# Kernel optimization log

Hardware: AMD Instinct MI355X
Metric: run time of the kernel (lower is better)

Reference implementation:

```python
import jax, jax.numpy as jnp
import numpy as np

B, T, C, H, W = 32, 64, 2, 32, 32
NK, KS = 16, 6          # n_kernels, kernel_size
ACT = 27                # conv output spatial size (32-6+1)
FEAT = ACT * ACT * NK   # 11664 flattened features
RU = 16                 # rnn_units
AD_RATE_L, REC_RATE_L = 0.1, 0.1   # AdaptiveLayer rates
AD_RATE_R, REC_RATE_R = 0.4, 0.1   # SimpleRNN rates


def setup_inputs() -> dict:
    key = jax.random.key(0)
    ks = jax.random.split(key, 8)
    stdv = 1.0 / np.sqrt(RU)
    return {
        "x": jax.random.normal(ks[0], (B, T, C, H, W), jnp.float32),
        "conv_w": jax.random.normal(ks[1], (NK, C, KS, KS), jnp.float32) * 0.01,
        "conv_b": jnp.full((NK,), 0.01, jnp.float32),
        "w_ih": jax.random.uniform(ks[2], (RU, FEAT), jnp.float32, -stdv, stdv),
        "w_hh": jax.random.uniform(ks[3], (RU, RU), jnp.float32, -stdv, stdv),
        "b_ih": jax.random.uniform(ks[4], (RU,), jnp.float32, -stdv, stdv),
        "b_hh": jax.random.uniform(ks[5], (RU,), jnp.float32, -stdv, stdv),
        "fc_w": jax.random.normal(ks[6], (2, RU), jnp.float32) * 0.01,
        "fc_b": jnp.full((2,), 0.01, jnp.float32),
    }


def reference(x, conv_w, conv_b, w_ih, w_hh, b_ih, b_hh, fc_w, fc_b):
    Bn, Tn = x.shape[:2]
    # per-frame conv: fold frames into batch
    xf = x.reshape(Bn * Tn, C, H, W)
    conv = jax.lax.conv_general_dilated(
        xf, conv_w, window_strides=(1, 1), padding='VALID',
        dimension_numbers=('NCHW', 'OIHW', 'NCHW'))
    conv = conv + conv_b[None, :, None, None]
    out_conv = conv.reshape(Bn, Tn, NK, ACT, ACT)
    out_flat = jax.nn.relu(out_conv.reshape(Bn, Tn, FEAT))

    # AdaptiveLayer: per-frame clamp/decay scan (initial adaptation is zeros)
    def ad_step(adapt, frame):
        out = jnp.maximum(frame - adapt, 0.0)
        adapt = (adapt + AD_RATE_L * out) * (1.0 - REC_RATE_L)
        return adapt, out
    _, adapted = jax.lax.scan(ad_step, jnp.zeros((Bn, FEAT), x.dtype),
                              jnp.swapaxes(out_flat, 0, 1))
    out_adapted = jnp.swapaxes(adapted, 0, 1)  # [B,T,FEAT]

    # SimpleRNN with adaptation state
    def rnn_step(carry, x_t):
        h, adapt = carry
        pre = x_t @ w_ih.T + b_ih + h @ w_hh.T + b_hh
        a = jnp.maximum(pre - adapt, 0.0)
        adapt = (adapt + AD_RATE_R * a) * (1.0 - REC_RATE_R)
        h = jax.nn.relu(a)
        return (h, adapt), h
    h0 = jnp.zeros((Bn, RU), x.dtype)
    _, hs = jax.lax.scan(rnn_step, (h0, h0), jnp.swapaxes(out_adapted, 0, 1))
    out_rnn = jnp.swapaxes(hs, 0, 1)  # [B,T,RU]

    out_fc = out_rnn @ fc_w.T + fc_b  # [B,T,2]
    return (out_fc, out_conv, out_flat, out_rnn)
```

## Files before the change

kernel.cpp:

```cpp
#include <hip/hip_runtime.h>

#define FEAT 11664
#define OFF_FC   0u
#define OFF_CONV 4096u
#define OFF_FLAT 23891968u
#define OFF_RNN  47779840u

static __device__ __forceinline__ unsigned short f2bf(float f) {
    unsigned int u = __float_as_uint(f);
    u += 0x7FFFu + ((u >> 16) & 1u);
    return (unsigned short)(u >> 16);
}

__global__ __launch_bounds__(128) void k_conv(const float* __restrict__ x,
                                              const float* __restrict__ cw,
                                              const float* __restrict__ cb,
                                              float* __restrict__ out)
{
    __shared__ __align__(16) float smem[11664];
    __shared__ float bls[16];
    float* xs  = smem;
    float* wls = smem + 2304;
    float* ot  = smem;
    const int tid = threadIdx.x;
    const int frame = blockIdx.x;

    const float4* xg = (const float4*)(x + (size_t)frame * 2048);
    for (int c0 = tid; c0 < 512; c0 += 128) {
        float4 v = xg[c0];
        int e0 = c0 * 4;
        int ch = e0 >> 10, rem = e0 & 1023, row = rem >> 5, col = rem & 31;
        float* dst = &xs[ch * 1152 + row * 36 + col];
        dst[0] = v.x; dst[1] = v.y; dst[2] = v.z; dst[3] = v.w;
    }
    for (int idx = tid; idx < 1152; idx += 128) {
        int k = idx / 72;
        int rem = idx - k * 72;
        wls[rem * 16 + k] = cw[idx];
    }
    if (tid < 16) bls[tid] = cb[tid];
    __syncthreads();

    const int kg = tid >> 5;
    const int r  = tid & 31;
    float acc[4][27];
    if (r < 27) {
        #pragma unroll
        for (int kk = 0; kk < 4; ++kk)
            #pragma unroll
            for (int c = 0; c < 27; ++c) acc[kk][c] = 0.f;

        for (int ch = 0; ch < 2; ++ch) {
            for (int i = 0; i < 6; ++i) {
                const float* rowp = &xs[ch * 1152 + (r + i) * 36];
                float xr[32];
                #pragma unroll
                for (int m = 0; m < 8; ++m) {
                    float4 v = ((const float4*)rowp)[m];
                    xr[4*m+0] = v.x; xr[4*m+1] = v.y; xr[4*m+2] = v.z; xr[4*m+3] = v.w;
                }
                float4 wj[6];
                #pragma unroll
                for (int j = 0; j < 6; ++j)
                    wj[j] = *(const float4*)&wls[(ch * 36 + i * 6 + j) * 16 + kg * 4];
                #pragma unroll
                for (int j = 0; j < 6; ++j) {
                    #pragma unroll
                    for (int c = 0; c < 27; ++c) {
                        float xv = xr[c + j];
                        acc[0][c] = fmaf(xv, wj[j].x, acc[0][c]);
                        acc[1][c] = fmaf(xv, wj[j].y, acc[1][c]);
                        acc[2][c] = fmaf(xv, wj[j].z, acc[2][c]);
                        acc[3][c] = fmaf(xv, wj[j].w, acc[3][c]);
                    }
                }
            }
        }
    }

    __syncthreads();
    if (r < 27) {
        #pragma unroll
        for (int kk = 0; kk < 4; ++kk) {
            float bv = bls[kg * 4 + kk];
            float* dst = &ot[(kg * 4 + kk) * 729 + r * 27];
            #pragma unroll
            for (int c = 0; c < 27; ++c) dst[c] = acc[kk][c] + bv;
        }
    }
    __syncthreads();

    const float4* src4 = (const float4*)ot;
    float4* dc = (float4*)(out + OFF_CONV + (size_t)frame * FEAT);
    float4* df = (float4*)(out + OFF_FLAT + (size_t)frame * FEAT);
    for (int e = tid; e < 2916; e += 128) {
        float4 v = src4[e];
        dc[e] = v;
        float4 rv;
        rv.x = v.x > 0.f ? v.x : 0.f;
        rv.y = v.y > 0.f ? v.y : 0.f;
        rv.z = v.z > 0.f ? v.z : 0.f;
        rv.w = v.w > 0.f ? v.w : 0.f;
        df[e] = rv;
    }
}

typedef short bf16x8 __attribute__((ext_vector_type(8)));
typedef float f32x4  __attribute__((ext_vector_type(4)));

__global__ __launch_bounds__(256) void k_adapt_proj48(const float* __restrict__ flat,
                                                      const float* __restrict__ w_ih,
                                                      float* __restrict__ partial)
{
    __shared__ __align__(16) unsigned short A[16 * 264];
    __shared__ __align__(16) unsigned short Bw[16 * 264];
    __shared__ __align__(16) float accscr[4 * 64 * 4];
    const int tid = threadIdx.x;
    const int b  = blockIdx.x / 48;
    const int fb = blockIdx.x % 48;
    const int fbase = fb * 243;

    float v[16];
    if (tid < 243) {
        const float* p0 = flat + (size_t)(b * 64) * FEAT + fbase + tid;
        #pragma unroll
        for (int tl = 0; tl < 16; ++tl) v[tl] = p0[(size_t)tl * FEAT];
    }

    for (int n = 0; n < 16; ++n) {
        if (tid < 243) Bw[n * 264 + tid] = f2bf(w_ih[(size_t)n * FEAT + fbase + tid]);
    }
    if (tid < 208) {
        int n = tid / 13, c = 243 + tid % 13;
        A[n * 264 + c]  = 0;
        Bw[n * 264 + c] = 0;
    }
    __syncthreads();

    float ad = 0.f;
    const int w = tid >> 6, l = tid & 63;
    const int m = l & 15, q = l >> 4;

    for (int tt = 0; tt < 4; ++tt) {
        if (tid < 243) {
            unsigned short* arow = &A[tid];
            #pragma unroll
            for (int tl = 0; tl < 16; ++tl) {
                float o = fmaxf(v[tl] - ad, 0.f); ad = (ad + 0.1f * o) * 0.9f;
                arow[tl * 264] = f2bf(o);
            }
        }
        __syncthreads();

        if (tt < 3 && tid < 243) {
            const float* pn = flat + (size_t)(b * 64 + (tt + 1) * 16) * FEAT + fbase + tid;
            #pragma unroll
            for (int tl = 0; tl < 16; ++tl) v[tl] = pn[(size_t)tl * FEAT];
        }

        f32x4 acc = {0.f, 0.f, 0.f, 0.f};
        #pragma unroll
        for (int s = w; s < 8; s += 4) {
            int k0 = s * 32;
            bf16x8 av = *(const bf16x8*)&A [m * 264 + k0 + q * 8];
            bf16x8 bv = *(const bf16x8*)&Bw[m * 264 + k0 + q * 8];
            acc = __builtin_amdgcn_mfma_f32_16x16x32_bf16(av, bv, acc, 0, 0, 0);
        }
        *(f32x4*)&accscr[(w * 64 + l) * 4] = acc;
        __syncthreads();
        {
            int ll = tid >> 2, rg = tid & 3;
            float s = accscr[(0 * 64 + ll) * 4 + rg] + accscr[(1 * 64 + ll) * 4 + rg]
                    + accscr[(2 * 64 + ll) * 4 + rg] + accscr[(3 * 64 + ll) * 4 + rg];
            int row = ((ll >> 4) * 4) + rg;
            int col = ll & 15;
            partial[(size_t)(((fb * 32 + b) * 64 + tt * 16 + row) * 16) + col] = s;
        }
        __syncthreads();
    }
}

__global__ __launch_bounds__(256) void k_adapt_proj16(const float* __restrict__ flat,
                                                      const float* __restrict__ w_ih,
                                                      float* __restrict__ partial)
{
    __shared__ __align__(16) unsigned short A[16 * 744];
    __shared__ __align__(16) unsigned short Bw[16 * 744];
    __shared__ __align__(16) float accscr[4 * 64 * 4];
    const int tid = threadIdx.x;
    const int b  = blockIdx.x >> 4;
    const int fb = blockIdx.x & 15;
    const int fbase = fb * 729;

    float v0[16], v1[16], v2[16];
    const float* src0 = flat + (size_t)(b * 64) * FEAT + fbase + tid * 3;
    if (tid < 243) {
        #pragma unroll
        for (int tl = 0; tl < 16; ++tl) {
            const float* p = src0 + (size_t)tl * FEAT;
            v0[tl] = p[0]; v1[tl] = p[1]; v2[tl] = p[2];
        }
    }

    for (int n = 0; n < 16; ++n) {
        const float* src = w_ih + (size_t)n * FEAT + fbase;
        for (int f = tid; f < 729; f += 256) Bw[n * 744 + f] = f2bf(src[f]);
    }
    if (tid < 240) {
        int n = tid / 15, c = 729 + (tid % 15);
        A[n * 744 + c]  = 0;
        Bw[n * 744 + c] = 0;
    }
    __syncthreads();

    float ad0 = 0.f, ad1 = 0.f, ad2 = 0.f;
    const int w = tid >> 6, l = tid & 63;
    const int m = l & 15, q = l >> 4;

    for (int tt = 0; tt < 4; ++tt) {
        if (tid < 243) {
            unsigned short* arow = &A[tid * 3];
            #pragma unroll
            for (int tl = 0; tl < 16; ++tl) {
                float o0 = fmaxf(v0[tl] - ad0, 0.f); ad0 = (ad0 + 0.1f * o0) * 0.9f;
                float o1 = fmaxf(v1[tl] - ad1, 0.f); ad1 = (ad1 + 0.1f * o1) * 0.9f;
                float o2 = fmaxf(v2[tl] - ad2, 0.f); ad2 = (ad2 + 0.1f * o2) * 0.9f;
                unsigned short* dst = arow + tl * 744;
                dst[0] = f2bf(o0); dst[1] = f2bf(o1); dst[2] = f2bf(o2);
            }
        }
        __syncthreads();

        if (tt < 3 && tid < 243) {
            const float* srcn = flat + (size_t)(b * 64 + (tt + 1) * 16) * FEAT + fbase + tid * 3;
            #pragma unroll
            for (int tl = 0; tl < 16; ++tl) {
                const float* p = srcn + (size_t)tl * FEAT;
                v0[tl] = p[0]; v1[tl] = p[1]; v2[tl] = p[2];
            }
        }

        f32x4 acc = {0.f, 0.f, 0.f, 0.f};
        for (int s = w; s < 23; s += 4) {
            int k0 = s * 32;
            bf16x8 av = *(const bf16x8*)&A [m * 744 + k0 + q * 8];
            bf16x8 bv = *(const bf16x8*)&Bw[m * 744 + k0 + q * 8];
            acc = __builtin_amdgcn_mfma_f32_16x16x32_bf16(av, bv, acc, 0, 0, 0);
        }
        *(f32x4*)&accscr[(w * 64 + l) * 4] = acc;
        __syncthreads();
        {
            int ll = tid >> 2, rg = tid & 3;
            float s = accscr[(0 * 64 + ll) * 4 + rg] + accscr[(1 * 64 + ll) * 4 + rg]
                    + accscr[(2 * 64 + ll) * 4 + rg] + accscr[(3 * 64 + ll) * 4 + rg];
            int row = ((ll >> 4) * 4) + rg;
            int col = ll & 15;
            partial[(size_t)(((fb * 32 + b) * 64 + tt * 16 + row) * 16) + col] = s;
        }
        __syncthreads();
    }
}

template<int NFB>
__global__ __launch_bounds__(64) void k_rnn_t(const float* __restrict__ partial,
                                              const float* __restrict__ w_hh,
                                              const float* __restrict__ b_ih,
                                              const float* __restrict__ b_hh,
                                              const float* __restrict__ fc_w,
                                              const float* __restrict__ fc_b,
                                              float* __restrict__ out)
{
    __shared__ __align__(16) float preL[4096];
    __shared__ float hL[64];
    const int l = threadIdx.x;
    const int bl = l >> 4, u = l & 15;
    const int b = blockIdx.x * 4 + bl;

    const float4* p4 = (const float4*)partial;
    float4* pl4 = (float4*)preL;
    for (int c = l; c < 1024; c += 64) {
        float4 s = {0.f, 0.f, 0.f, 0.f};
        for (int fb = 0; fb < NFB; ++fb) {
            float4 v = p4[(size_t)fb * 8192 + blockIdx.x * 1024 + c];
            s.x += v.x; s.y += v.y; s.z += v.z; s.w += v.w;
        }
        pl4[c] = s;
    }

    float wv[16];
    #pragma unroll
    for (int mm = 0; mm < 4; ++mm) {
        float4 t4 = *(const float4*)(w_hh + u * 16 + mm * 4);
        wv[4*mm+0] = t4.x; wv[4*mm+1] = t4.y; wv[4*mm+2] = t4.z; wv[4*mm+3] = t4.w;
    }
    const float bsum = b_ih[u] + b_hh[u];
    float frow[16]; float fcb = 0.f;
    if (u < 2) {
        #pragma unroll
        for (int mm = 0; mm < 4; ++mm) {
            float4 t4 = *(const float4*)(fc_w + u * 16 + mm * 4);
            frow[4*mm+0] = t4.x; frow[4*mm+1] = t4.y; frow[4*mm+2] = t4.z; frow[4*mm+3] = t4.w;
        }
        fcb = fc_b[u];
    }
    hL[l] = 0.f;
    float ad = 0.f;

    for (int t = 0; t < 64; ++t) {
        float hv[16];
        #pragma unroll
        for (int mm = 0; mm < 4; ++mm) {
            float4 h4 = *(const float4*)&hL[bl * 16 + mm * 4];
            hv[4*mm+0] = h4.x; hv[4*mm+1] = h4.y; hv[4*mm+2] = h4.z; hv[4*mm+3] = h4.w;
        }
        if (t > 0 && u < 2) {
            float fcv = fcb;
            #pragma unroll
            for (int v2 = 0; v2 < 16; ++v2) fcv = fmaf(hv[v2], frow[v2], fcv);
            out[OFF_FC + (size_t)(b * 64 + (t - 1)) * 2 + u] = fcv;
        }
        float dot = 0.f;
        #pragma unroll
        for (int v2 = 0; v2 < 16; ++v2) dot = fmaf(hv[v2], wv[v2], dot);
        float v = preL[(bl * 64 + t) * 16 + u] + bsum + dot;
        float a = v - ad; a = a > 0.f ? a : 0.f;
        ad = (ad + 0.4f * a) * 0.9f;
        out[OFF_RNN + (size_t)(b * 64 + t) * 16 + u] = a;
        hL[l] = a;
    }
    {
        float hv[16];
        #pragma unroll
        for (int mm = 0; mm < 4; ++mm) {
            float4 h4 = *(const float4*)&hL[bl * 16 + mm * 4];
            hv[4*mm+0] = h4.x; hv[4*mm+1] = h4.y; hv[4*mm+2] = h4.z; hv[4*mm+3] = h4.w;
        }
        if (u < 2) {
            float fcv = fcb;
            #pragma unroll
            for (int v2 = 0; v2 < 16; ++v2) fcv = fmaf(hv[v2], frow[v2], fcv);
            out[OFF_FC + (size_t)(b * 64 + 63) * 2 + u] = fcv;
        }
    }
}

extern "C" void kernel_launch(void* const* d_in, const int* in_sizes, int n_in,
                              void* d_out, int out_size, void* d_ws, size_t ws_size,
                              hipStream_t stream)
{
    const float* x    = (const float*)d_in[0];
    const float* cw   = (const float*)d_in[1];
    const float* cb   = (const float*)d_in[2];
    const float* w_ih = (const float*)d_in[3];
    const float* w_hh = (const float*)d_in[4];
    const float* b_ih = (const float*)d_in[5];
    const float* b_hh = (const float*)d_in[6];
    const float* fc_w = (const float*)d_in[7];
    const float* fc_b = (const float*)d_in[8];
    float* out = (float*)d_out;
    float* partial = (float*)d_ws;

    k_conv<<<2048, 128, 0, stream>>>(x, cw, cb, out);

    const size_t need48 = 48ull * 32 * 64 * 16 * 4;
    if (ws_size >= need48) {
        k_adapt_proj48<<<1536, 256, 0, stream>>>(out + OFF_FLAT, w_ih, partial);
        k_rnn_t<48><<<8, 64, 0, stream>>>(partial, w_hh, b_ih, b_hh, fc_w, fc_b, out);
    } else {
        k_adapt_proj16<<<512, 256, 0, stream>>>(out + OFF_FLAT, w_ih, partial);
        k_rnn_t<16><<<8, 64, 0, stream>>>(partial, w_hh, b_ih, b_hh, fc_w, fc_b, out);
    }
}
```

Baseline: 316.2 us.

## Pre-convert w_ih to bf16 in conv kernel, hold B fragments in registers, parallelize reduction

The w_ih fp32→bf16 conversion moves into 16 extra blocks of the conv kernel, which write a padded bf16 layout to workspace. The projection kernel then loads its MFMA B fragments straight into registers, so each of the 1536 blocks no longer reconverts w_ih through LDS, and one barrier per iteration is dropped. The 48-way partial-sum reduction, previously done serially inside the 8-block RNN kernel, moves into a separate 128-block reduce kernel. This adds one kernel launch and relies on a larger workspace being available.

```diff
diff --git a/kernel.cpp b/kernel.cpp
--- a/kernel.cpp
+++ b/kernel.cpp
@@ -15,15 +15,30 @@
 __global__ __launch_bounds__(128) void k_conv(const float* __restrict__ x,
                                               const float* __restrict__ cw,
                                               const float* __restrict__ cb,
-                                              float* __restrict__ out)
+                                              float* __restrict__ out,
+                                              const float* __restrict__ w_ih,
+                                              unsigned short* __restrict__ wb,
+                                              int cvt)
 {
     __shared__ __align__(16) float smem[11664];
     __shared__ float bls[16];
+    const int tid = threadIdx.x;
+
+    if (blockIdx.x < (unsigned)cvt) {
+        const int n = blockIdx.x;
+        const float* src = w_ih + (size_t)n * FEAT;
+        for (int idx = tid; idx < 48 * 264; idx += 128) {
+            int fb = idx / 264, c = idx - fb * 264;
+            unsigned short v = (c < 243) ? f2bf(src[fb * 243 + c]) : (unsigned short)0;
+            wb[(size_t)(fb * 16 + n) * 264 + c] = v;
+        }
+        return;
+    }
+
     float* xs  = smem;
     float* wls = smem + 2304;
     float* ot  = smem;
-    const int tid = threadIdx.x;
-    const int frame = blockIdx.x;
+    const int frame = blockIdx.x - cvt;
 
     const float4* xg = (const float4*)(x + (size_t)frame * 2048);
     for (int c0 = tid; c0 < 512; c0 += 128) {
@@ -109,37 +124,36 @@
 typedef float f32x4  __attribute__((ext_vector_type(4)));
 
 __global__ __launch_bounds__(256) void k_adapt_proj48(const float* __restrict__ flat,
-                                                      const float* __restrict__ w_ih,
+                                                      const unsigned short* __restrict__ wb,
                                                       float* __restrict__ partial)
 {
     __shared__ __align__(16) unsigned short A[16 * 264];
-    __shared__ __align__(16) unsigned short Bw[16 * 264];
     __shared__ __align__(16) float accscr[4 * 64 * 4];
     const int tid = threadIdx.x;
     const int b  = blockIdx.x / 48;
     const int fb = blockIdx.x % 48;
     const int fbase = fb * 243;
 
+    const int w = tid >> 6, l = tid & 63;
+    const int m = l & 15, q = l >> 4;
+
+    const unsigned short* wbp = wb + (size_t)(fb * 16) * 264;
+    bf16x8 bf0 = *(const bf16x8*)&wbp[m * 264 + (w    ) * 32 + q * 8];
+    bf16x8 bf1 = *(const bf16x8*)&wbp[m * 264 + (w + 4) * 32 + q * 8];
+
     float v[16];
     if (tid < 243) {
         const float* p0 = flat + (size_t)(b * 64) * FEAT + fbase + tid;
         #pragma unroll
         for (int tl = 0; tl < 16; ++tl) v[tl] = p0[(size_t)tl * FEAT];
     }
-
-    for (int n = 0; n < 16; ++n) {
-        if (tid < 243) Bw[n * 264 + tid] = f2bf(w_ih[(size_t)n * FEAT + fbase + tid]);
-    }
     if (tid < 208) {
         int n = tid / 13, c = 243 + tid % 13;
-        A[n * 264 + c]  = 0;
-        Bw[n * 264 + c] = 0;
+        A[n * 264 + c] = 0;
     }
     __syncthreads();
 
     float ad = 0.f;
-    const int w = tid >> 6, l = tid & 63;
-    const int m = l & 15, q = l >> 4;
 
     for (int tt = 0; tt < 4; ++tt) {
         if (tid < 243) {
@@ -159,12 +173,11 @@
         }
 
         f32x4 acc = {0.f, 0.f, 0.f, 0.f};
-        #pragma unroll
-        for (int s = w; s < 8; s += 4) {
-            int k0 = s * 32;
-            bf16x8 av = *(const bf16x8*)&A [m * 264 + k0 + q * 8];
-            bf16x8 bv = *(const bf16x8*)&Bw[m * 264 + k0 + q * 8];
-            acc = __builtin_amdgcn_mfma_f32_16x16x32_bf16(av, bv, acc, 0, 0, 0);
+        {
+            bf16x8 a0 = *(const bf16x8*)&A[m * 264 + (w    ) * 32 + q * 8];
+            acc = __builtin_amdgcn_mfma_f32_16x16x32_bf16(a0, bf0, acc, 0, 0, 0);
+            bf16x8 a1 = *(const bf16x8*)&A[m * 264 + (w + 4) * 32 + q * 8];
+            acc = __builtin_amdgcn_mfma_f32_16x16x32_bf16(a1, bf1, acc, 0, 0, 0);
         }
         *(f32x4*)&accscr[(w * 64 + l) * 4] = acc;
         __syncthreads();
@@ -176,7 +189,6 @@
             int col = ll & 15;
             partial[(size_t)(((fb * 32 + b) * 64 + tt * 16 + row) * 16) + col] = s;
         }
-        __syncthreads();
     }
 }
 
@@ -261,8 +273,96 @@
     }
 }
 
-template<int NFB>
-__global__ __launch_bounds__(64) void k_rnn_t(const float* __restrict__ partial,
+__global__ __launch_bounds__(256) void k_reduce(const float* __restrict__ partial,
+                                                float* __restrict__ pre)
+{
+    const int idx = blockIdx.x * 256 + threadIdx.x;
+    const float4* p4 = (const float4*)partial;
+    float4 s = {0.f, 0.f, 0.f, 0.f};
+    #pragma unroll
+    for (int fb = 0; fb < 48; ++fb) {
+        float4 v = p4[(size_t)fb * 8192 + idx];
+        s.x += v.x; s.y += v.y; s.z += v.z; s.w += v.w;
+    }
+    ((float4*)pre)[idx] = s;
+}
+
+__global__ __launch_bounds__(64) void k_rnn_pre(const float* __restrict__ pre,
+                                                const float* __restrict__ w_hh,
+                                                const float* __restrict__ b_ih,
+                                                const float* __restrict__ b_hh,
+                                                const float* __restrict__ fc_w,
+                                                const float* __restrict__ fc_b,
+                                                float* __restrict__ out)
+{
+    __shared__ __align__(16) float preL[4096];
+    __shared__ float hL[64];
+    const int l = threadIdx.x;
+    const int bl = l >> 4, u = l & 15;
+    const int b = blockIdx.x * 4 + bl;
+
+    const float4* p4 = (const float4*)pre;
+    float4* pl4 = (float4*)preL;
+    for (int c = l; c < 1024; c += 64) pl4[c] = p4[(size_t)blockIdx.x * 1024 + c];
+
+    float wv[16];
+    #pragma unroll
+    for (int mm = 0; mm < 4; ++mm) {
+        float4 t4 = *(const float4*)(w_hh + u * 16 + mm * 4);
+        wv[4*mm+0] = t4.x; wv[4*mm+1] = t4.y; wv[4*mm+2] = t4.z; wv[4*mm+3] = t4.w;
+    }
+    const float bsum = b_ih[u] + b_hh[u];
+    float frow[16]; float fcb = 0.f;
+    if (u < 2) {
+        #pragma unroll
+        for (int mm = 0; mm < 4; ++mm) {
+            float4 t4 = *(const float4*)(fc_w + u * 16 + mm * 4);
+            frow[4*mm+0] = t4.x; frow[4*mm+1] = t4.y; frow[4*mm+2] = t4.z; frow[4*mm+3] = t4.w;
+        }
+        fcb = fc_b[u];
+    }
+    hL[l] = 0.f;
+    float ad = 0.f;
+
+    for (int t = 0; t < 64; ++t) {
+        float hv[16];
+        #pragma unroll
+        for (int mm = 0; mm < 4; ++mm) {
+            float4 h4 = *(const float4*)&hL[bl * 16 + mm * 4];
+            hv[4*mm+0] = h4.x; hv[4*mm+1] = h4.y; hv[4*mm+2] = h4.z; hv[4*mm+3] = h4.w;
+        }
+        if (t > 0 && u < 2) {
+            float fcv = fcb;
+            #pragma unroll
+            for (int v2 = 0; v2 < 16; ++v2) fcv = fmaf(hv[v2], frow[v2], fcv);
+            out[OFF_FC + (size_t)(b * 64 + (t - 1)) * 2 + u] = fcv;
+        }
+        float dot = 0.f;
+        #pragma unroll
+        for (int v2 = 0; v2 < 16; ++v2) dot = fmaf(hv[v2], wv[v2], dot);
+        float v = preL[(bl * 64 + t) * 16 + u] + bsum + dot;
+        float a = v - ad; a = a > 0.f ? a : 0.f;
+        ad = (ad + 0.4f * a) * 0.9f;
+        out[OFF_RNN + (size_t)(b * 64 + t) * 16 + u] = a;
+        hL[l] = a;
+    }
+    {
+        float hv[16];
+        #pragma unroll
+        for (int mm = 0; mm < 4; ++mm) {
+            float4 h4 = *(const float4*)&hL[bl * 16 + mm * 4];
+            hv[4*mm+0] = h4.x; hv[4*mm+1] = h4.y; hv[4*mm+2] = h4.z; hv[4*mm+3] = h4.w;
+        }
+        if (u < 2) {
+            float fcv = fcb;
+            #pragma unroll
+            for (int v2 = 0; v2 < 16; ++v2) fcv = fmaf(hv[v2], frow[v2], fcv);
+            out[OFF_FC + (size_t)(b * 64 + 63) * 2 + u] = fcv;
+        }
+    }
+}
+
+__global__ __launch_bounds__(64) void k_rnn16(const float* __restrict__ partial,
                                               const float* __restrict__ w_hh,
                                               const float* __restrict__ b_ih,
                                               const float* __restrict__ b_hh,
@@ -280,7 +380,7 @@
     float4* pl4 = (float4*)preL;
     for (int c = l; c < 1024; c += 64) {
         float4 s = {0.f, 0.f, 0.f, 0.f};
-        for (int fb = 0; fb < NFB; ++fb) {
+        for (int fb = 0; fb < 16; ++fb) {
             float4 v = p4[(size_t)fb * 8192 + blockIdx.x * 1024 + c];
             s.x += v.x; s.y += v.y; s.z += v.z; s.w += v.w;
         }
@@ -358,16 +458,23 @@
     const float* fc_w = (const float*)d_in[7];
     const float* fc_b = (const float*)d_in[8];
     float* out = (float*)d_out;
+
+    const size_t off_wb  = 6291456;
+    const size_t off_pre = off_wb + 405504;
+    const size_t need    = off_pre + 524288;
+
     float* partial = (float*)d_ws;
 
-    k_conv<<<2048, 128, 0, stream>>>(x, cw, cb, out);
-
-    const size_t need48 = 48ull * 32 * 64 * 16 * 4;
-    if (ws_size >= need48) {
-        k_adapt_proj48<<<1536, 256, 0, stream>>>(out + OFF_FLAT, w_ih, partial);
-        k_rnn_t<48><<<8, 64, 0, stream>>>(partial, w_hh, b_ih, b_hh, fc_w, fc_b, out);
+    if (ws_size >= need) {
+        unsigned short* wb = (unsigned short*)((char*)d_ws + off_wb);
+        float* pre = (float*)((char*)d_ws + off_pre);
+        k_conv<<<2064, 128, 0, stream>>>(x, cw, cb, out, w_ih, wb, 16);
+        k_adapt_proj48<<<1536, 256, 0, stream>>>(out + OFF_FLAT, wb, partial);
+        k_reduce<<<128, 256, 0, stream>>>(partial, pre);
+        k_rnn_pre<<<8, 64, 0, stream>>>(pre, w_hh, b_ih, b_hh, fc_w, fc_b, out);
     } else {
+        k_conv<<<2048, 128, 0, stream>>>(x, cw, cb, out, w_ih, nullptr, 0);
         k_adapt_proj16<<<512, 256, 0, stream>>>(out + OFF_FLAT, w_ih, partial);
-        k_rnn_t<16><<<8, 64, 0, stream>>>(partial, w_hh, b_ih, b_hh, fc_w, fc_b, out);
-    }
-}
+        k_rnn16<<<8, 64, 0, stream>>>(partial, w_hh, b_ih, b_hh, fc_w, fc_b, out);
+    }
+}
```

Measured after the change: 298.0 us. 5.8% less time.
